# Kernel optimization log

Measured on AMD Instinct MI355X. Metric: run time of the kernel, lower is better.

## Reference

```python
import jax, jax.numpy as jnp
from jax import lax
import numpy as np

B, T, I, H = 8192, 365, 3, 34


def setup_inputs() -> dict:
    key = jax.random.key(0)
    ks = jax.random.split(key, 7)
    s_in = 1.0 / np.sqrt(I)
    s_h = 1.0 / np.sqrt(H)
    return {
        "x": jax.random.normal(ks[0], (B, T, I), dtype=jnp.float32),
        "fc0_w": jax.random.uniform(ks[1], (H, I), jnp.float32, -s_in, s_in),
        "fc0_b": jax.random.uniform(ks[2], (H,), jnp.float32, -s_in, s_in),
        "w_ih": jax.random.uniform(ks[3], (4 * H, H), jnp.float32, -s_h, s_h),
        "w_hh": jax.random.uniform(ks[4], (4 * H, H), jnp.float32, -s_h, s_h),
        "b_ih": jax.random.uniform(ks[5], (4 * H,), jnp.float32, -s_h, s_h),
        "b_hh": jax.random.uniform(ks[6], (4 * H,), jnp.float32, -s_h, s_h),
    }


def reference(x, fc0_w, fc0_b, w_ih, w_hh, b_ih, b_hh):
    # fc0: [B,T,I] -> [B,T,H]
    l1 = jnp.einsum("bti,hi->bth", x, fc0_w) + fc0_b
    # Precompute input-side gate projections for all timesteps: [B,T,4H]
    gx = jnp.einsum("bth,gh->btg", l1, w_ih) + b_ih + b_hh
    gx_t = jnp.swapaxes(gx, 0, 1)  # [T,B,4H]

    h0 = jnp.zeros((x.shape[0], fc0_w.shape[0]), dtype=x.dtype)
    c0 = h0

    def step(carry, g_t):
        h, c = carry
        gates = g_t + h @ w_hh.T  # [B,4H]
        i, f, g, o = jnp.split(gates, 4, axis=-1)  # torch gate order: i,f,g,o
        i = jax.nn.sigmoid(i)
        f = jax.nn.sigmoid(f)
        g = jnp.tanh(g)
        o = jax.nn.sigmoid(o)
        c_new = f * c + i * g
        h_new = o * jnp.tanh(c_new)
        return (h_new, c_new), h_new

    (_, _), hs = lax.scan(step, (h0, c0), gx_t)  # hs: [T,B,H]
    return jnp.swapaxes(hs, 0, 1)  # [B,T,H]
```

## Files before the change

### kernel.cpp

```cpp
#include <hip/hip_runtime.h>

namespace {

constexpr int Bn = 8192;
constexpr int Tn = 365;
constexpr int Hn = 34;
constexpr int GB = 16;
constexpr int KP = 104;
constexpr int GS = 44;

constexpr float L2E = 1.44269504088896340736f;

typedef __attribute__((ext_vector_type(8))) short bf16x8;
typedef __attribute__((ext_vector_type(4))) float f32x4;

__device__ __forceinline__ float fexp2(float v) { return __builtin_amdgcn_exp2f(v); }
__device__ __forceinline__ float frcp(float v)  { return __builtin_amdgcn_rcpf(v); }

__device__ __forceinline__ unsigned short f2bf(float f) {
    union { float f; unsigned u; } v; v.f = f;
    unsigned r = v.u + 0x7fffu + ((v.u >> 16) & 1u);
    return (unsigned short)(r >> 16);
}
__device__ __forceinline__ float bf2f(unsigned short s) {
    union { unsigned u; float f; } v; v.u = ((unsigned)s) << 16; return v.f;
}
__device__ __forceinline__ unsigned packh(float h) {
    unsigned short hh = f2bf(h);
    unsigned short hl = f2bf(h - bf2f(hh));
    return (unsigned)hh | ((unsigned)hl << 16);
}

__device__ __forceinline__ void lds_fence() {
    __builtin_amdgcn_sched_barrier(0);
    asm volatile("s_waitcnt lgkmcnt(0)" ::: "memory");
    __builtin_amdgcn_sched_barrier(0);
}
__device__ __forceinline__ void block_sync_lds() {
    __builtin_amdgcn_sched_barrier(0);
    asm volatile("s_waitcnt lgkmcnt(0)" ::: "memory");
    __builtin_amdgcn_s_barrier();
    __builtin_amdgcn_sched_barrier(0);
}


__global__ __launch_bounds__(256) void lstm_kernel(
    const float* __restrict__ x,
    const float* __restrict__ fc0_w,
    const float* __restrict__ fc0_b,
    const float* __restrict__ w_ih,
    const float* __restrict__ w_hh,
    const float* __restrict__ b_ih,
    const float* __restrict__ b_hh,
    float* __restrict__ out)
{
    __shared__ __align__(16) unsigned short a_lds[2][GB][KP];
    __shared__ __align__(16) float g_lds[4][GB][GS];

    const int tid  = threadIdx.x;
    const int lane = tid & 63;
    const int wv   = tid >> 6;
    const int c    = lane & 15;
    const int kg   = lane >> 4;

    const int nc   = (wv < 2) ? 9 : 8;
    const int base = (wv < 2) ? 9 * wv : 18 + 8 * (wv - 2);

    bf16x8 Bt[3][3];
    #pragma unroll
    for (int tau = 0; tau < 3; ++tau) {
        const int rhat = 16 * tau + c;
        const int jl = rhat >> 2, g = rhat & 3;
        const int r = (rhat < 4 * nc) ? g * Hn + (base + jl) : -1;
        const float s = (g == 2) ? (2.f * L2E) : (-L2E);
        float wcv[3] = {0.f, 0.f, 0.f};
        float bia = 0.f;
        if (r >= 0) {
            float ab = 0.f;
            for (int m = 0; m < Hn; ++m) {
                const float wi = w_ih[r * Hn + m];
                wcv[0] += wi * fc0_w[m * 3 + 0];
                wcv[1] += wi * fc0_w[m * 3 + 1];
                wcv[2] += wi * fc0_w[m * 3 + 2];
                ab     += wi * fc0_b[m];
            }
            wcv[0] *= s; wcv[1] *= s; wcv[2] *= s;
            bia = s * (ab + b_ih[r] + b_hh[r]);
        }
        #pragma unroll
        for (int ks = 0; ks < 3; ++ks) {
            bf16x8 f;
            #pragma unroll
            for (int e = 0; e < 8; ++e) {
                const int k = ks * 32 + kg * 8 + e;
                float val = 0.f;
                if (r >= 0) {
                    if (k < 68)       val = s * w_hh[r * Hn + (k >> 1)];
                    else if (k < 71)  val = wcv[k - 68];
                    else if (k < 74)  val = wcv[k - 71];
                    else if (k < 77)  { const float w = wcv[k - 74]; val = w - bf2f(f2bf(w)); }
                    else if (k == 77) val = bia;
                    else if (k == 78) val = bia - bf2f(f2bf(bia));
                }
                f[e] = (short)f2bf(val);
            }
            Bt[tau][ks] = f;
        }
    }

    const bool isg2 = ((c & 3) == 2);
    const float ku = isg2 ? -2.f : 1.f;
    const float kc = isg2 ?  1.f : 0.f;

    const int ub = c;
    const bool has2 = (nc == 9) && (kg == 0);
    float c0 = 0.f, c1 = 0.f, c2 = 0.f;
    float h0 = 0.f, h1 = 0.f, h2 = 0.f;

    const bool xact = (lane < 12);
    const int bx = 4 * wv + lane / 3;
    const int ix = lane - 3 * (lane / 3);

    for (int i = tid; i < 2 * GB * KP; i += 256) ((unsigned short*)a_lds)[i] = 0;
    block_sync_lds();

    const long long bg = (long long)blockIdx.x * GB;
    const float* xblk = x + bg * (long long)(Tn * 3);
    float* oblk = out + bg * (long long)(Tn * Hn);
    const long long TH = (long long)Tn * Hn;

    if (tid < 32) {
        a_lds[tid >> 4][tid & 15][77] = (unsigned short)0x3F80;
        a_lds[tid >> 4][tid & 15][78] = (unsigned short)0x3F80;
    }
    if (xact) {
        const float xr = xblk[bx * (Tn * 3) + ix];
        const unsigned short xh = f2bf(xr);
        a_lds[0][bx][68 + ix] = xh;
        a_lds[0][bx][71 + ix] = f2bf(xr - bf2f(xh));
        a_lds[0][bx][74 + ix] = xh;
    }
    block_sync_lds();

    for (int t = 0; t < Tn; ++t) {
        const int cur = t & 1, nxt = cur ^ 1;

        if (t) {
            const long long tb = (long long)ub * TH + (long long)(t - 1) * Hn + base;
            oblk[tb + kg]     = h0;
            oblk[tb + 4 + kg] = h1;
            if (has2) oblk[tb + 8] = h2;
        }
        float xr = 0.f;
        if (xact && t + 1 < Tn)
            xr = xblk[bx * (Tn * 3) + (t + 1) * 3 + ix];

        bf16x8 av[3];
        #pragma unroll
        for (int ks = 0; ks < 3; ++ks)
            av[ks] = *(const bf16x8*)(&a_lds[cur][c][ks * 32 + kg * 8]);

        f32x4 acc[3];
        #pragma unroll
        for (int tau = 0; tau < 3; ++tau) {
            acc[tau] = f32x4{0.f, 0.f, 0.f, 0.f};
            #pragma unroll
            for (int ks = 0; ks < 3; ++ks)
                acc[tau] = __builtin_amdgcn_mfma_f32_16x16x32_bf16(av[ks], Bt[tau][ks], acc[tau], 0, 0, 0);
        }

        #pragma unroll
        for (int tau = 0; tau < 3; ++tau) {
            #pragma unroll
            for (int p = 0; p < 4; ++p) {
                const float e2 = fexp2(acc[tau][p]);
                const float u  = frcp(1.f + e2);
                const float gv = fmaf(ku, u, kc);
                if (16 * tau + c < 4 * nc)
                    g_lds[wv][4 * kg + p][16 * tau + c] = gv;
            }
        }

        lds_fence();

        {
            const f32x4 gv = *(const f32x4*)&g_lds[wv][ub][4 * kg];
            c0 = gv[1] * c0 + gv[0] * gv[2];
            h0 = gv[3] * fmaf(-2.f, frcp(1.f + fexp2(c0 * (2.f * L2E))), 1.f);
            ((unsigned*)&a_lds[nxt][ub][0])[base + kg] = packh(h0);
        }
        {
            const f32x4 gv = *(const f32x4*)&g_lds[wv][ub][4 * (4 + kg)];
            c1 = gv[1] * c1 + gv[0] * gv[2];
            h1 = gv[3] * fmaf(-2.f, frcp(1.f + fexp2(c1 * (2.f * L2E))), 1.f);
            ((unsigned*)&a_lds[nxt][ub][0])[base + 4 + kg] = packh(h1);
        }
        if (has2) {
            const f32x4 gv = *(const f32x4*)&g_lds[wv][ub][4 * 8];
            c2 = gv[1] * c2 + gv[0] * gv[2];
            h2 = gv[3] * fmaf(-2.f, frcp(1.f + fexp2(c2 * (2.f * L2E))), 1.f);
            ((unsigned*)&a_lds[nxt][ub][0])[base + 8] = packh(h2);
        }

        if (xact) {
            const unsigned short xh = f2bf(xr);
            a_lds[nxt][bx][68 + ix] = xh;
            a_lds[nxt][bx][71 + ix] = f2bf(xr - bf2f(xh));
            a_lds[nxt][bx][74 + ix] = xh;
        }

        block_sync_lds();
    }

    {
        const long long tb = (long long)ub * TH + (long long)(Tn - 1) * Hn + base;
        oblk[tb + kg]     = h0;
        oblk[tb + 4 + kg] = h1;
        if (has2) oblk[tb + 8] = h2;
    }
}

}

extern "C" void kernel_launch(void* const* d_in, const int* in_sizes, int n_in,
                              void* d_out, int out_size, void* d_ws, size_t ws_size,
                              hipStream_t stream) {
    const float* x     = (const float*)d_in[0];
    const float* fc0_w = (const float*)d_in[1];
    const float* fc0_b = (const float*)d_in[2];
    const float* w_ih  = (const float*)d_in[3];
    const float* w_hh  = (const float*)d_in[4];
    const float* b_ih  = (const float*)d_in[5];
    const float* b_hh  = (const float*)d_in[6];
    float* out = (float*)d_out;

    lstm_kernel<<<Bn / GB, 256, 0, stream>>>(x, fc0_w, fc0_b, w_ih, w_hh, b_ih, b_hh, out);
}
```

Baseline: 409.4 us.

## Swap MFMA operands so each lane holds all four gates, removing gate LDS round-trip

Transposes the MFMA so weights are the A operand and hidden state the B operand. Each lane's accumulator then holds the i,f,g,o gates for one hidden unit and batch element. This removes the per-step write of activated gates to a shared LDS buffer, the LDS fence and the read-back, so the cell update runs directly from registers. The cost is that the third tile still computes all gates on the lanes the has2 guard masks off, and gate activations now run only on lanes that need them.

```diff
diff --git a/kernel.cpp b/kernel.cpp
--- a/kernel.cpp
+++ b/kernel.cpp
@@ -7,7 +7,6 @@
 constexpr int Hn = 34;
 constexpr int GB = 16;
 constexpr int KP = 104;
-constexpr int GS = 44;
 
 constexpr float L2E = 1.44269504088896340736f;
 
@@ -31,11 +30,6 @@
     return (unsigned)hh | ((unsigned)hl << 16);
 }
 
-__device__ __forceinline__ void lds_fence() {
-    __builtin_amdgcn_sched_barrier(0);
-    asm volatile("s_waitcnt lgkmcnt(0)" ::: "memory");
-    __builtin_amdgcn_sched_barrier(0);
-}
 __device__ __forceinline__ void block_sync_lds() {
     __builtin_amdgcn_sched_barrier(0);
     asm volatile("s_waitcnt lgkmcnt(0)" ::: "memory");
@@ -55,23 +49,22 @@
     float* __restrict__ out)
 {
     __shared__ __align__(16) unsigned short a_lds[2][GB][KP];
-    __shared__ __align__(16) float g_lds[4][GB][GS];
 
     const int tid  = threadIdx.x;
     const int lane = tid & 63;
     const int wv   = tid >> 6;
-    const int c    = lane & 15;
+    const int b    = lane & 15;
     const int kg   = lane >> 4;
 
     const int nc   = (wv < 2) ? 9 : 8;
     const int base = (wv < 2) ? 9 * wv : 18 + 8 * (wv - 2);
 
-    bf16x8 Bt[3][3];
+    bf16x8 Wt[3][3];
     #pragma unroll
     for (int tau = 0; tau < 3; ++tau) {
-        const int rhat = 16 * tau + c;
+        const int rhat = 16 * tau + b;
         const int jl = rhat >> 2, g = rhat & 3;
-        const int r = (rhat < 4 * nc) ? g * Hn + (base + jl) : -1;
+        const int r = (jl < nc) ? g * Hn + (base + jl) : -1;
         const float s = (g == 2) ? (2.f * L2E) : (-L2E);
         float wcv[3] = {0.f, 0.f, 0.f};
         float bia = 0.f;
@@ -104,16 +97,11 @@
                 }
                 f[e] = (short)f2bf(val);
             }
-            Bt[tau][ks] = f;
-        }
-    }
-
-    const bool isg2 = ((c & 3) == 2);
-    const float ku = isg2 ? -2.f : 1.f;
-    const float kc = isg2 ?  1.f : 0.f;
-
-    const int ub = c;
-    const bool has2 = (nc == 9) && (kg == 0);
+            Wt[tau][ks] = f;
+        }
+    }
+
+    const bool has2 = (8 + kg < nc);
     float c0 = 0.f, c1 = 0.f, c2 = 0.f;
     float h0 = 0.f, h1 = 0.f, h2 = 0.f;
 
@@ -146,10 +134,10 @@
         const int cur = t & 1, nxt = cur ^ 1;
 
         if (t) {
-            const long long tb = (long long)ub * TH + (long long)(t - 1) * Hn + base;
+            const long long tb = (long long)b * TH + (long long)(t - 1) * Hn + base;
             oblk[tb + kg]     = h0;
             oblk[tb + 4 + kg] = h1;
-            if (has2) oblk[tb + 8] = h2;
+            if (has2) oblk[tb + 8 + kg] = h2;
         }
         float xr = 0.f;
         if (xact && t + 1 < Tn)
@@ -158,7 +146,7 @@
         bf16x8 av[3];
         #pragma unroll
         for (int ks = 0; ks < 3; ++ks)
-            av[ks] = *(const bf16x8*)(&a_lds[cur][c][ks * 32 + kg * 8]);
+            av[ks] = *(const bf16x8*)(&a_lds[cur][b][ks * 32 + kg * 8]);
 
         f32x4 acc[3];
         #pragma unroll
@@ -166,40 +154,35 @@
             acc[tau] = f32x4{0.f, 0.f, 0.f, 0.f};
             #pragma unroll
             for (int ks = 0; ks < 3; ++ks)
-                acc[tau] = __builtin_amdgcn_mfma_f32_16x16x32_bf16(av[ks], Bt[tau][ks], acc[tau], 0, 0, 0);
-        }
-
-        #pragma unroll
-        for (int tau = 0; tau < 3; ++tau) {
-            #pragma unroll
-            for (int p = 0; p < 4; ++p) {
-                const float e2 = fexp2(acc[tau][p]);
-                const float u  = frcp(1.f + e2);
-                const float gv = fmaf(ku, u, kc);
-                if (16 * tau + c < 4 * nc)
-                    g_lds[wv][4 * kg + p][16 * tau + c] = gv;
-            }
-        }
-
-        lds_fence();
+                acc[tau] = __builtin_amdgcn_mfma_f32_16x16x32_bf16(Wt[tau][ks], av[ks], acc[tau], 0, 0, 0);
+        }
 
         {
-            const f32x4 gv = *(const f32x4*)&g_lds[wv][ub][4 * kg];
-            c0 = gv[1] * c0 + gv[0] * gv[2];
-            h0 = gv[3] * fmaf(-2.f, frcp(1.f + fexp2(c0 * (2.f * L2E))), 1.f);
-            ((unsigned*)&a_lds[nxt][ub][0])[base + kg] = packh(h0);
+            const float gi = frcp(1.f + fexp2(acc[0][0]));
+            const float gf = frcp(1.f + fexp2(acc[0][1]));
+            const float gg = fmaf(-2.f, frcp(1.f + fexp2(acc[0][2])), 1.f);
+            const float go = frcp(1.f + fexp2(acc[0][3]));
+            c0 = gf * c0 + gi * gg;
+            h0 = go * fmaf(-2.f, frcp(1.f + fexp2(c0 * (2.f * L2E))), 1.f);
+            ((unsigned*)&a_lds[nxt][b][0])[base + kg] = packh(h0);
         }
         {
-            const f32x4 gv = *(const f32x4*)&g_lds[wv][ub][4 * (4 + kg)];
-            c1 = gv[1] * c1 + gv[0] * gv[2];
-            h1 = gv[3] * fmaf(-2.f, frcp(1.f + fexp2(c1 * (2.f * L2E))), 1.f);
-            ((unsigned*)&a_lds[nxt][ub][0])[base + 4 + kg] = packh(h1);
+            const float gi = frcp(1.f + fexp2(acc[1][0]));
+            const float gf = frcp(1.f + fexp2(acc[1][1]));
+            const float gg = fmaf(-2.f, frcp(1.f + fexp2(acc[1][2])), 1.f);
+            const float go = frcp(1.f + fexp2(acc[1][3]));
+            c1 = gf * c1 + gi * gg;
+            h1 = go * fmaf(-2.f, frcp(1.f + fexp2(c1 * (2.f * L2E))), 1.f);
+            ((unsigned*)&a_lds[nxt][b][0])[base + 4 + kg] = packh(h1);
         }
         if (has2) {
-            const f32x4 gv = *(const f32x4*)&g_lds[wv][ub][4 * 8];
-            c2 = gv[1] * c2 + gv[0] * gv[2];
-            h2 = gv[3] * fmaf(-2.f, frcp(1.f + fexp2(c2 * (2.f * L2E))), 1.f);
-            ((unsigned*)&a_lds[nxt][ub][0])[base + 8] = packh(h2);
+            const float gi = frcp(1.f + fexp2(acc[2][0]));
+            const float gf = frcp(1.f + fexp2(acc[2][1]));
+            const float gg = fmaf(-2.f, frcp(1.f + fexp2(acc[2][2])), 1.f);
+            const float go = frcp(1.f + fexp2(acc[2][3]));
+            c2 = gf * c2 + gi * gg;
+            h2 = go * fmaf(-2.f, frcp(1.f + fexp2(c2 * (2.f * L2E))), 1.f);
+            ((unsigned*)&a_lds[nxt][b][0])[base + 8 + kg] = packh(h2);
         }
 
         if (xact) {
@@ -213,10 +196,10 @@
     }
 
     {
-        const long long tb = (long long)ub * TH + (long long)(Tn - 1) * Hn + base;
+        const long long tb = (long long)b * TH + (long long)(Tn - 1) * Hn + base;
         oblk[tb + kg]     = h0;
         oblk[tb + 4 + kg] = h1;
-        if (has2) oblk[tb + 8] = h2;
+        if (has2) oblk[tb + 8 + kg] = h2;
     }
 }
 
```

Result: faster. 370.6 us (-9.5%).
